# Performance work log

Hardware: AMD Instinct MI355X
Metric: run time of the kernel (lower is better)

## Reference

```python
import jax, jax.numpy as jnp
import numpy as np
import math
from jax import lax


def _pos_enc(C, T, V, dtype):
    # spatial positional encoding: position = joint index j for every (t, j)
    pos = jnp.tile(jnp.arange(V, dtype=dtype), T)[:, None]            # (T*V, 1)
    div = jnp.exp(jnp.arange(0, C, 2, dtype=dtype) * (-(math.log(10000.0) / C)))
    ang = pos * div                                                   # (T*V, C//2)
    pe = jnp.stack([jnp.sin(ang), jnp.cos(ang)], axis=-1).reshape(T * V, C)
    return pe.reshape(T, V, C).transpose(2, 0, 1)[None]               # (1, C, T, V)


def _sparsemax(z, axis):
    z = jnp.moveaxis(z, axis, -1)
    K = z.shape[-1]
    zs = jnp.flip(jnp.sort(z, axis=-1), axis=-1)                      # descending
    cs = jnp.cumsum(zs, axis=-1)
    k = jnp.arange(1, K + 1, dtype=z.dtype)
    support = (1.0 + k * zs) > cs
    ks = jnp.sum(support, axis=-1, keepdims=True)                     # support size (int)
    tau = (jnp.take_along_axis(cs, ks - 1, axis=-1) - 1.0) / ks.astype(z.dtype)
    out = jnp.maximum(z - tau, 0.0)
    return jnp.moveaxis(out, -1, axis)


def _conv2d(x, w, b, pad_h=0, stride_h=1):
    out = lax.conv_general_dilated(x, w, (stride_h, 1), ((pad_h, pad_h), (0, 0)),
                                   dimension_numbers=('NCHW', 'OIHW', 'NCHW'))
    return out + b.reshape(1, -1, 1, 1)


def _bn(x, g, be, m, v, eps=1e-5):
    inv = g / jnp.sqrt(v + eps)
    return x * inv.reshape(1, -1, 1, 1) + (be - m * inv).reshape(1, -1, 1, 1)


def reference(x, theta, atts, alphas, v_w, v_b, out_w, out_b, out_g, out_be, out_m, out_v,
              ff_w, ff_b, ff_g, ff_be, ff_m, ff_v):
    N, C, T, V = x.shape
    S = theta.shape[1]

    # positional encoding + kernel attention
    y = x + _pos_enc(C, T, V, x.dtype)
    yf = y.transpose(0, 3, 1, 2).reshape(N, V, C * T)                 # (N, V, C*T)
    sq = jnp.sum(yf * yf, axis=-1)
    d2 = sq[:, :, None] + sq[:, None, :] - 2.0 * jnp.einsum('nvd,nud->nvu', yf, yf)
    d2 = jnp.maximum(d2, 0.0)                                         # cdist^2
    dism = d2 / float((C * T) ** 2)                                   # (d / (C*T))^2
    dism = dism / jnp.max(dism)
    kernel_atten = jnp.exp(-jnp.exp(theta) * dism[:, None])           # (N, S, V, V)
    kernel_atten = _sparsemax(kernel_atten, axis=-2)                  # sparsity_alpha == 2
    attention = atts + kernel_atten * alphas                          # is_regularization=True; dropout in eval

    # value mapping (1x1 conv) + subset aggregation
    vx = jnp.einsum('oc,nctv->notv', v_w.reshape(v_w.shape[0], v_w.shape[1]), x) + v_b.reshape(1, -1, 1, 1)
    y = jnp.einsum('nctu,nsuv->nsctv', vx, attention).reshape(N, S * C, T, V)

    # out_nets: temporal conv (k,1) + BN
    pad = (out_w.shape[2] - 1) // 2
    y = _bn(_conv2d(y, out_w, out_b, pad_h=pad), out_g, out_be, out_m, out_v)
    y = jax.nn.leaky_relu(x + y, negative_slope=0.1)                  # downs1 = identity

    # ff_nets: 1x1 conv + BN
    y2 = _bn(_conv2d(y, ff_w, ff_b), ff_g, ff_be, ff_m, ff_v)
    return jax.nn.leaky_relu(x + y2, negative_slope=0.1)              # downs2 = identity


def setup_inputs() -> dict:
    key = jax.random.key(0)
    ks = jax.random.split(key, 8)
    N, C, T, V, S, K = 64, 128, 128, 25, 3, 7
    Cout = 128
    inp = {}
    inp['x'] = jax.random.normal(ks[0], (N, C, T, V), dtype=jnp.float32)
    inp['theta'] = jax.random.normal(ks[1], (1, S, 1, 1), dtype=jnp.float32) * 0.1
    inp['atts'] = jax.random.normal(ks[2], (1, S, V, V), dtype=jnp.float32) * 0.1
    inp['alphas'] = jnp.ones((1, S, 1, 1), dtype=jnp.float32)
    inp['v_w'] = jax.random.normal(ks[3], (C, C, 1, 1), dtype=jnp.float32) * (1.0 / math.sqrt(C))
    inp['v_b'] = jax.random.normal(ks[4], (C,), dtype=jnp.float32) * 0.01
    inp['out_w'] = jax.random.normal(ks[5], (Cout, S * C, K, 1), dtype=jnp.float32) * (1.0 / math.sqrt(S * C * K))
    inp['out_b'] = jax.random.normal(ks[6], (Cout,), dtype=jnp.float32) * 0.01
    inp['out_g'] = jnp.ones((Cout,), dtype=jnp.float32)
    inp['out_be'] = jnp.zeros((Cout,), dtype=jnp.float32)
    inp['out_m'] = jnp.zeros((Cout,), dtype=jnp.float32)
    inp['out_v'] = jnp.ones((Cout,), dtype=jnp.float32)
    inp['ff_w'] = jax.random.normal(ks[7], (Cout, Cout, 1, 1), dtype=jnp.float32) * (1.0 / math.sqrt(Cout))
    inp['ff_b'] = jnp.zeros((Cout,), dtype=jnp.float32)
    inp['ff_g'] = jnp.ones((Cout,), dtype=jnp.float32)
    inp['ff_be'] = jnp.zeros((Cout,), dtype=jnp.float32)
    inp['ff_m'] = jnp.zeros((Cout,), dtype=jnp.float32)
    inp['ff_v'] = jnp.ones((Cout,), dtype=jnp.float32)
    return inp
```

## Files before the change

### kernel.cpp

```cpp
#include <hip/hip_runtime.h>
#include <hip/hip_bf16.h>
#include <math.h>

typedef __attribute__((ext_vector_type(8))) short s16x8;
typedef __attribute__((ext_vector_type(4))) float f32x4;

static __device__ __forceinline__ float bf2f(unsigned short u){
    unsigned int x = ((unsigned int)u) << 16; float f; __builtin_memcpy(&f,&x,4); return f;
}
static __device__ __forceinline__ unsigned short f2bf(float f){
    unsigned int x; __builtin_memcpy(&x,&f,4);
    unsigned int r = (x + 0x7FFFu + ((x>>16)&1u)) >> 16; return (unsigned short)r;
}

static __device__ __forceinline__ void stage16(const void* g, void* l){
    __builtin_amdgcn_global_load_lds((const __attribute__((address_space(1))) unsigned int*)g,
                                     (__attribute__((address_space(3))) unsigned int*)l, 16, 0, 0);
}


__global__ __launch_bounds__(256) void setup_kernel(const float* __restrict__ x,
                            const float* __restrict__ out_w, const float* __restrict__ ff_w,
                            const float* __restrict__ v_w,  const float* __restrict__ v_b,
                            const float* __restrict__ out_b, const float* __restrict__ out_g,
                            const float* __restrict__ out_be, const float* __restrict__ out_m,
                            const float* __restrict__ out_v,
                            const float* __restrict__ ff_b, const float* __restrict__ ff_g,
                            const float* __restrict__ ff_be, const float* __restrict__ ff_m,
                            const float* __restrict__ ff_v,
                            float* __restrict__ consts, unsigned short* __restrict__ ffA,
                            unsigned short* __restrict__ ypad, float* __restrict__ wbpart,
                            float* __restrict__ pebg, float* __restrict__ TPgb,
                            unsigned short* __restrict__ Wr,
                            unsigned short* __restrict__ xbt, unsigned short* __restrict__ xbu,
                            float* __restrict__ G, float* __restrict__ SX)
{
    __shared__ float tile[64][65];
    const int bid = blockIdx.x;
    const int tid = threadIdx.x;

    if (bid < 6400){
        int jb = bid % 50; int cb = (bid/50) & 1; int n = bid/100;
        int lane = tid & 63, wv = tid >> 6;
        size_t xbase = (size_t)n*409600;
        int jn = jb*64 + lane;
        int tt = jn/25, uu = jn - tt*25;
        size_t xbu_lb = (size_t)n*524288 + (size_t)tt*4096 + uu;
        #pragma unroll
        for (int r=wv; r<64; r+=4){
            float v = x[xbase + (size_t)(cb*64+r)*3200 + jb*64 + lane];
            tile[r][lane] = v;
            xbu[xbu_lb + (size_t)(cb*64+r)*32] = f2bf(v);
        }
        __syncthreads();
        #pragma unroll
        for (int j=wv; j<64; j+=4)
            xbt[xbase + (size_t)(jb*64+j)*128 + cb*64 + lane] = f2bf(tile[lane][j]);
        return;
    }

    if (bid < 7296){
        float* owl = &tile[0][0];
        int wb = bid - 6400;
        int o = wb/7, k = wb%7;
        for (int i=tid; i<384; i+=256) owl[i] = out_w[(size_t)(o*384 + i)*7 + k];
        __syncthreads();
        for (int sci=tid; sci<384; sci+=256){
            int s = sci >> 7, ci = sci & 127;
            const float* ow = owl + s*128;
            float acc = 0.f;
            #pragma unroll 8
            for (int c=0; c<128; ++c) acc += ow[c] * v_w[c*128 + ci];
            int kb = (sci>>5)*7 + k, jj = sci & 31;
            Wr[(size_t)o*2688 + kb*32 + jj] = f2bf(acc);
        }
        return;
    }

    const int stride = 2048*256;
    int i0 = (bid-7296)*256 + tid;
    const float KLN = 9.210340371976184f/128.f;
    for (int i=i0; i<40000;  i+=stride) G[i]  = 0.f;
    for (int i=i0; i<204800; i+=stride) SX[i] = 0.f;
    for (int i=i0; i<16384; i+=stride) ffA[i] = f2bf(ff_w[i]);
    for (int i=i0; i<128; i+=stride){
        float inv  = out_g[i]/sqrtf(out_v[i]+1e-5f);
        consts[i]       = inv;
        consts[128+i]   = out_b[i]*inv + out_be[i] - out_m[i]*inv;
        float invf = ff_g[i]/sqrtf(ff_v[i]+1e-5f);
        consts[256+i]   = invf;
        consts[384+i]   = ff_b[i]*invf + ff_be[i] - ff_m[i]*invf;
    }
    for (int i=i0; i<3200; i+=stride){
        int v = i >> 7, c = i & 127;
        float freq = expf(-(float)(c & ~1) * KLN);
        float ang = (float)v * freq;
        pebg[i] = (c & 1) ? cosf(ang) : sinf(ang);
    }
    for (int i=i0; i<625; i+=stride){
        int u = i/25, v = i%25;
        float acc = 0.f;
        for (int c=0; c<128; ++c){
            float freq = expf(-(float)(c & ~1) * KLN);
            float pu = (c & 1) ? cosf((float)u*freq) : sinf((float)u*freq);
            float pv = (c & 1) ? cosf((float)v*freq) : sinf((float)v*freq);
            acc += pu*pv;
        }
        TPgb[i] = 128.f*acc;
    }
    for (int i=i0; i<2688; i+=stride){
        int o = i/21, rem = i%21, s = rem/7, tc = rem%7;
        int kmin = (tc<3) ? (3-tc) : 0;
        int kmax = (tc>3) ? (10-tc) : 7;
        float acc = 0.f;
        for (int c=0; c<128; ++c){
            const float* wp = out_w + (size_t)(o*384 + s*128 + c)*7;
            float vb = v_b[c];
            for (int k=kmin; k<kmax; ++k) acc += wp[k]*vb;
        }
        wbpart[i] = acc;
    }
    for (int i=i0; i<3686400; i+=stride){
        int n2 = i/57600, r2 = i%57600;
        int pp = r2/384, sc = r2%384;
        int ppos = (pp < 75) ? pp : (3200 + pp);
        ypad[(size_t)(n2*3350 + ppos)*384 + sc] = 0;
    }
}

__global__ __launch_bounds__(256) void gram_part(const unsigned short* __restrict__ xbt,
                                                 float* __restrict__ G, float* __restrict__ SX){
    __shared__ float glx[4][32][32];
    int bid = blockIdx.x; int n = bid >> 3; int chunk = bid & 7;
    int tid = threadIdx.x;
    const unsigned short* xb = xbt + (size_t)n*409600;

    int c = tid & 127, th = tid >> 7;
    float a[25];
    #pragma unroll
    for (int u=0; u<25; ++u) a[u] = 0.f;
    for (int tt=0; tt<8; ++tt){
        int t = chunk*16 + th*8 + tt;
        const unsigned short* row = xb + (size_t)t*3200 + c;
        #pragma unroll
        for (int u=0; u<25; ++u) a[u] += bf2f(row[u*128]);
    }
    float* tmp = &glx[0][0][0];
    if (th){
        #pragma unroll
        for (int u=0; u<25; ++u) tmp[u*128+c] = a[u];
    }
    __syncthreads();
    if (!th){
        #pragma unroll
        for (int u=0; u<25; ++u) atomicAdd(&SX[n*3200 + u*128 + c], a[u] + tmp[u*128+c]);
    }
    __syncthreads();

    int lane = tid & 63, w = tid >> 6;
    int lr = lane & 15, lg = lane >> 4;
    f32x4 acc[2][2];
    #pragma unroll
    for (int i2=0;i2<2;i2++)
        #pragma unroll
        for (int j2=0;j2<2;j2++) acc[i2][j2] = (f32x4){0.f,0.f,0.f,0.f};
    for (int tt=0; tt<4; ++tt){
        int t = chunk*16 + w*4 + tt;
        const unsigned short* tb = xb + (size_t)t*3200;
        #pragma unroll
        for (int kc=0; kc<4; ++kc){
            s16x8 f0 = *(const s16x8*)(tb + (size_t)(lr)*128    + kc*32 + lg*8);
            s16x8 f1 = *(const s16x8*)(tb + (size_t)(16+lr)*128 + kc*32 + lg*8);
            acc[0][0] = __builtin_amdgcn_mfma_f32_16x16x32_bf16(f0, f0, acc[0][0], 0,0,0);
            acc[0][1] = __builtin_amdgcn_mfma_f32_16x16x32_bf16(f0, f1, acc[0][1], 0,0,0);
            acc[1][0] = __builtin_amdgcn_mfma_f32_16x16x32_bf16(f1, f0, acc[1][0], 0,0,0);
            acc[1][1] = __builtin_amdgcn_mfma_f32_16x16x32_bf16(f1, f1, acc[1][1], 0,0,0);
        }
    }
    #pragma unroll
    for (int mh=0; mh<2; ++mh)
        #pragma unroll
        for (int nh=0; nh<2; ++nh)
            #pragma unroll
            for (int r=0; r<4; ++r)
                glx[w][mh*16 + lg*4 + r][nh*16 + lr] = acc[mh][nh][r];
    __syncthreads();
    for (int idx=tid; idx<625; idx+=256){
        int u = idx/25, v = idx%25;
        atomicAdd(&G[n*625 + idx], glx[0][u][v] + glx[1][u][v] + glx[2][u][v] + glx[3][u][v]);
    }
}

__global__ __launch_bounds__(256) void gram_fin(const float* __restrict__ SX,
                                                const float* __restrict__ pebg,
                                                const float* __restrict__ TPgb,
                                                float* __restrict__ G,
                                                float* __restrict__ nmax){
    __shared__ float sxl[25][129];
    __shared__ float pebl[25][129];
    __shared__ float gf[625];
    __shared__ float red[256];
    int n = blockIdx.x, tid = threadIdx.x;
    for (int i=tid; i<3200; i+=256){
        sxl[i>>7][i&127]  = SX[n*3200 + i];
        pebl[i>>7][i&127] = pebg[i];
    }
    __syncthreads();
    for (int idx=tid; idx<625; idx+=256){
        int u = idx/25, v = idx%25;
        float cr = TPgb[idx];
        #pragma unroll 4
        for (int cc=0; cc<128; ++cc)
            cr += sxl[u][cc]*pebl[v][cc] + sxl[v][cc]*pebl[u][cc];
        float val = G[n*625 + idx] + cr;
        G[n*625 + idx] = val;
        gf[idx] = val;
    }
    __syncthreads();
    float mx = 0.f;
    for (int idx=tid; idx<625; idx+=256){
        int u = idx/25, v = idx%25;
        float d2 = fmaxf(gf[u*26] + gf[v*26] - 2.f*gf[u*25+v], 0.f);
        mx = fmaxf(mx, d2);
    }
    red[tid] = mx; __syncthreads();
    for (int s2=128; s2>0; s2>>=1){ if (tid < s2) red[tid] = fmaxf(red[tid], red[tid+s2]); __syncthreads(); }
    if (tid == 0) nmax[n] = red[0];
}

__global__ __launch_bounds__(128) void attn_kernel(const float* __restrict__ G, const float* __restrict__ nmax,
                                                   const float* __restrict__ theta,
                                                   const float* __restrict__ atts, const float* __restrict__ alphas,
                                                   unsigned short* __restrict__ att_pad, float* __restrict__ asum){
    __shared__ float gl[625];
    __shared__ float red[64];
    int n = blockIdx.x, tid = threadIdx.x;
    if (tid < 64) red[tid] = nmax[tid];
    for (int i=tid; i<625; i+=128) gl[i] = G[n*625 + i];
    __syncthreads();
    if (tid == 0){
        float m = red[0];
        for (int i=1; i<64; ++i) m = fmaxf(m, red[i]);
        red[0] = m;
    }
    __syncthreads();
    float inv = 1.f/red[0];
    for (int i=tid; i<160; i+=128) att_pad[n*2560 + 2400 + i] = 0;
    if (tid < 75){
        int s = tid/25, vc = tid%25;
        float et = expf(theta[s]);
        float al = alphas[s];
        float gvv = gl[vc*26];
        float z[25];
        #pragma unroll
        for (int u2=0; u2<25; ++u2){
            float d2v = fmaxf(gl[u2*26] + gvv - 2.f*gl[u2*25+vc], 0.f);
            z[u2] = expf(-et*d2v*inv);
        }
        float zm = z[0];
        #pragma unroll
        for (int u2=1; u2<25; ++u2) zm = fmaxf(zm, z[u2]);
        float lo = zm - 1.f, hi = zm;
        for (int it=0; it<30; ++it){
            float mid = 0.5f*(lo+hi);
            float f = 0.f;
            #pragma unroll
            for (int u2=0; u2<25; ++u2) f += fmaxf(z[u2]-mid, 0.f);
            if (f >= 1.f) lo = mid; else hi = mid;
        }
        float ssum = 0.f; int kcnt = 0;
        #pragma unroll
        for (int u2=0; u2<25; ++u2){ if (z[u2] > lo){ ssum += z[u2]; kcnt++; } }
        float tau = (ssum - 1.f)/(float)kcnt;
        float as_ = 0.f;
        unsigned short* apr = att_pad + n*2560 + (s*25+vc)*32;
        #pragma unroll
        for (int u2=0; u2<25; ++u2){
            float av = atts[s*625 + u2*25 + vc] + fmaxf(z[u2]-tau, 0.f)*al;
            apr[u2] = f2bf(av);
            as_ += av;
        }
        #pragma unroll
        for (int u2=25; u2<32; ++u2) apr[u2] = 0;
        asum[n*75 + s*25 + vc] = as_;
    }
}

__global__ __launch_bounds__(256,2) void agg_mfma(const unsigned short* __restrict__ att_pad,
                                                  const unsigned short* __restrict__ xbu,
                                                  unsigned short* __restrict__ ypad){
    int bid = blockIdx.x; int n = bid >> 4; int tb = bid & 15;
    int tid = threadIdx.x; int lane = tid & 63; int w = tid >> 6;
    int lr = lane & 15, lg = lane >> 4;
    const unsigned short* ap = att_pad + n*2560;
    s16x8 a[5];
    #pragma unroll
    for (int mf=0; mf<5; ++mf) a[mf] = *(const s16x8*)&ap[(mf*16+lr)*32 + lg*8];
    int rowoff[5][4];
    #pragma unroll
    for (int mf=0; mf<5; ++mf)
        #pragma unroll
        for (int r=0; r<4; ++r){
            int m = mf*16 + lg*4 + r;
            int s = m/25, v = m - s*25;
            rowoff[mf][r] = (m < 75) ? (v*384 + s*128 + lr) : -1;
        }
    #pragma unroll
    for (int ti=0; ti<2; ++ti){
        int t = tb*8 + w*2 + ti;
        const unsigned short* bp = xbu + (size_t)n*524288 + (size_t)t*4096;
        size_t obase = ((size_t)(n*3350 + 75 + t*25))*384;
        #pragma unroll
        for (int h=0; h<2; ++h){
            s16x8 b[4];
            #pragma unroll
            for (int q=0; q<4; ++q){
                b[q] = *(const s16x8*)&bp[(h*64 + q*16 + lr)*32 + lg*8];
                if (lg == 3){
                    s16x8 t2 = b[q];
                    b[q] = (s16x8){t2[0],0,0,0,0,0,0,0};
                }
            }
            f32x4 acc[5][4];
            #pragma unroll
            for (int mf=0; mf<5; ++mf)
                #pragma unroll
                for (int q=0; q<4; ++q)
                    acc[mf][q] = (f32x4){0.f,0.f,0.f,0.f};
            #pragma unroll
            for (int mf=0; mf<5; ++mf)
                #pragma unroll
                for (int q=0; q<4; ++q)
                    acc[mf][q] = __builtin_amdgcn_mfma_f32_16x16x32_bf16(a[mf], b[q], acc[mf][q], 0, 0, 0);
            #pragma unroll
            for (int mf=0; mf<5; ++mf)
                #pragma unroll
                for (int q=0; q<4; ++q)
                    #pragma unroll
                    for (int r=0; r<4; ++r)
                        if (rowoff[mf][r] >= 0)
                            ypad[obase + rowoff[mf][r] + h*64 + q*16] = f2bf(acc[mf][q][r]);
        }
    }
}

__global__ __launch_bounds__(256,3) void gemm_fused(const unsigned short* __restrict__ Amat,
                                                    const unsigned short* __restrict__ Bsrc,
                                                    const float* __restrict__ xin,
                                                    const float* __restrict__ consts,
                                                    const unsigned short* __restrict__ ffA,
                                                    const float* __restrict__ wbpart,
                                                    const float* __restrict__ asum,
                                                    float* __restrict__ outf)
{
    constexpr int NKB = 42;
    __shared__ unsigned short smem[17560];

    const int tid = threadIdx.x;
    const int bid = blockIdx.x;
    const int n   = bid/25;
    const int jn0 = (bid%25)*128;

    const int lane = tid & 63, wv = tid >> 6;
    const int wm = wv >> 1, wn = wv & 1;
    const int lr = lane & 15, lg = lane >> 4;

    unsigned short* sA = smem;
    unsigned short* sB = smem + 8192;

    auto stage = [&](int kb){
        #pragma unroll
        for (int p=0; p<4; ++p){
            int e = p*256 + tid;
            int r = e >> 3, cch = e & 7;
            int cc8 = cch ^ (r & 7);
            stage16(Amat + (size_t)r*2688 + kb*64 + cc8*8, sA + e*8);
        }
        int k32a = 2*kb, k32b = 2*kb + 1;
        int k0 = k32a % 7, s0 = (k32a/7)*32;
        int k1 = k32b % 7, s1 = (k32b/7)*32;
        const unsigned short* b0 = Bsrc + ((size_t)(n*3350 + jn0 + 25*k0))*384 + s0;
        const unsigned short* b1 = Bsrc + ((size_t)(n*3350 + jn0 + 25*k1))*384 + s1;
        #pragma unroll
        for (int p=0; p<4; ++p){
            int e = p*256 + tid;
            int r = e >> 3, cch = e & 7;
            int cc8 = cch ^ (r & 7);
            const unsigned short* src = ((cc8 >> 2) ? b1 : b0) + (size_t)r*384 + (cc8&3)*8;
            stage16(src, sB + e*8);
        }
    };

    f32x4 acc[4][4];
    #pragma unroll
    for (int a2=0;a2<4;a2++)
        #pragma unroll
        for (int b2=0;b2<4;b2++) acc[a2][b2] = (f32x4){0.f,0.f,0.f,0.f};

    for (int kb=0; kb<NKB; ++kb){
        stage(kb);
        __syncthreads();
        s16x8 a[4][2], b[4][2];
        #pragma unroll
        for (int mf=0; mf<4; ++mf)
            #pragma unroll
            for (int kf=0; kf<2; ++kf)
                a[mf][kf] = *(const s16x8*)&sA[(wm*64+mf*16+lr)*64 + (((kf*4+lg) ^ (lr&7))<<3)];
        #pragma unroll
        for (int nf=0; nf<4; ++nf)
            #pragma unroll
            for (int kf=0; kf<2; ++kf)
                b[nf][kf] = *(const s16x8*)&sB[(wn*64+nf*16+lr)*64 + (((kf*4+lg) ^ (lr&7))<<3)];
        __builtin_amdgcn_s_setprio(1);
        #pragma unroll
        for (int kf=0; kf<2; ++kf)
            #pragma unroll
            for (int mf=0; mf<4; ++mf)
                #pragma unroll
                for (int nf=0; nf<4; ++nf)
                    acc[mf][nf] = __builtin_amdgcn_mfma_f32_16x16x32_bf16(a[mf][kf], b[nf][kf], acc[mf][nf], 0, 0, 0);
        __builtin_amdgcn_s_setprio(0);
        __syncthreads();
    }

    float* asl = (float*)(smem + 17408);
    for (int i=tid; i<75; i+=256) asl[i] = asum[n*75 + i];
    __syncthreads();

    #pragma unroll
    for (int nf=0; nf<4; ++nf){
        int cj = wn*64 + nf*16 + lr;
        int j  = jn0 + cj;
        int t  = j/25, v = j - t*25;
        int tc = (t<3) ? t : ((t>124) ? (t-121) : 3);
        float a0 = asl[v], a1 = asl[25+v], a2 = asl[50+v];
        #pragma unroll
        for (int mf=0; mf<4; ++mf)
            #pragma unroll
            for (int r=0; r<4; ++r){
                int m = wm*64 + mf*16 + lg*4 + r;
                float b2v = wbpart[m*21+tc]*a0 + wbpart[m*21+7+tc]*a1 + wbpart[m*21+14+tc]*a2;
                float val = acc[mf][nf][r]*consts[m] + consts[128+m] + b2v
                          + xin[(size_t)n*409600 + (size_t)m*3200 + j];
                val = (val >= 0.f) ? val : 0.1f*val;
                smem[cj*136 + m] = f2bf(val);
            }
    }
    __syncthreads();

    f32x4 acc2[4][4];
    #pragma unroll
    for (int a2=0;a2<4;a2++)
        #pragma unroll
        for (int b2=0;b2<4;b2++) acc2[a2][b2] = (f32x4){0.f,0.f,0.f,0.f};
    #pragma unroll
    for (int kb2=0; kb2<4; ++kb2){
        s16x8 a2[4], b2[4];
        #pragma unroll
        for (int mf=0; mf<4; ++mf)
            a2[mf] = *(const s16x8*)&ffA[(size_t)(wm*64+mf*16+lr)*128 + kb2*32 + lg*8];
        #pragma unroll
        for (int nf=0; nf<4; ++nf)
            b2[nf] = *(const s16x8*)&smem[(wn*64+nf*16+lr)*136 + kb2*32 + lg*8];
        #pragma unroll
        for (int mf=0; mf<4; ++mf)
            #pragma unroll
            for (int nf=0; nf<4; ++nf)
                acc2[mf][nf] = __builtin_amdgcn_mfma_f32_16x16x32_bf16(a2[mf], b2[nf], acc2[mf][nf], 0, 0, 0);
    }

    #pragma unroll
    for (int mf=0; mf<4; ++mf)
        #pragma unroll
        for (int r=0; r<4; ++r){
            int co = wm*64 + mf*16 + lg*4 + r;
            float sc2 = consts[256+co], bi2 = consts[384+co];
            #pragma unroll
            for (int nf=0; nf<4; ++nf){
                int cj = wn*64 + nf*16 + lr;
                size_t idx = (size_t)n*409600 + (size_t)co*3200 + jn0 + cj;
                float val = acc2[mf][nf][r]*sc2 + bi2 + xin[idx];
                val = (val >= 0.f) ? val : 0.1f*val;
                outf[idx] = val;
            }
        }
}

extern "C" void kernel_launch(void* const* d_in, const int* in_sizes, int n_in,
                              void* d_out, int out_size, void* d_ws, size_t ws_size,
                              hipStream_t stream) {
    const float* x      = (const float*)d_in[0];
    const float* theta  = (const float*)d_in[1];
    const float* atts   = (const float*)d_in[2];
    const float* alphas = (const float*)d_in[3];
    const float* v_w    = (const float*)d_in[4];
    const float* v_b    = (const float*)d_in[5];
    const float* out_w  = (const float*)d_in[6];
    const float* out_b  = (const float*)d_in[7];
    const float* out_g  = (const float*)d_in[8];
    const float* out_be = (const float*)d_in[9];
    const float* out_m  = (const float*)d_in[10];
    const float* out_v  = (const float*)d_in[11];
    const float* ff_w   = (const float*)d_in[12];
    const float* ff_b   = (const float*)d_in[13];
    const float* ff_g   = (const float*)d_in[14];
    const float* ff_be  = (const float*)d_in[15];
    const float* ff_m   = (const float*)d_in[16];
    const float* ff_v   = (const float*)d_in[17];
    float* out = (float*)d_out;

    char* w = (char*)d_ws;
    size_t off = 0;
    auto alloc = [&](size_t b){ size_t r = off; off += (b + 1023) & ~(size_t)1023; return r; };
    float*          G      = (float*)         (w + alloc(160000));
    float*          SX     = (float*)         (w + alloc(819200));
    float*          nmaxb  = (float*)         (w + alloc(256));
    float*          asumb  = (float*)         (w + alloc(19200));
    float*          consts = (float*)         (w + alloc(2048));
    float*          wbpart = (float*)         (w + alloc(10752));
    float*          pebg   = (float*)         (w + alloc(12800));
    float*          TPgb   = (float*)         (w + alloc(2500));
    unsigned short* att_pad= (unsigned short*)(w + alloc(327680));
    unsigned short* Wr     = (unsigned short*)(w + alloc(688128));
    unsigned short* ffA    = (unsigned short*)(w + alloc(32768));
    unsigned short* xbt    = (unsigned short*)(w + alloc(52428800 + 16384));
    unsigned short* xbu    = (unsigned short*)(w + alloc(67108864));
    unsigned short* ypad   = (unsigned short*)(w + alloc(164659200));

    setup_kernel<<<9344,256,0,stream>>>(x, out_w, ff_w, v_w, v_b, out_b, out_g, out_be, out_m, out_v,
                                        ff_b, ff_g, ff_be, ff_m, ff_v,
                                        consts, ffA, ypad, wbpart, pebg, TPgb, Wr, xbt, xbu, G, SX);
    gram_part<<<512,256,0,stream>>>(xbt, G, SX);
    gram_fin<<<64,256,0,stream>>>(SX, pebg, TPgb, G, nmaxb);
    attn_kernel<<<64,128,0,stream>>>(G, nmaxb, theta, atts, alphas, att_pad, asumb);
    agg_mfma<<<1024,256,0,stream>>>(att_pad, xbu, ypad);
    gemm_fused<<<1600,256,0,stream>>>(Wr, ypad, x, consts, ffA, wbpart, asumb, out);
}
```

Before: 492.7 us.

## Load MFMA operands directly from global memory instead of staging through LDS

The GEMM main loop stops staging A and B tiles into shared memory with global_load_lds and barriers. Each lane now loads its MFMA fragments straight from global memory into registers, and the loop is unrolled by two. This removes LDS traffic and the two __syncthreads per k-step. In exchange, operands that the four waves used to share through LDS are now fetched from global memory redundantly, which relies on L1/L2 hits, and the loads are less coalesced (16-byte chunks spread across strided rows).

New measurement: 833.0 us. +69.1%, slower.

```diff
diff --git a/kernel.cpp b/kernel.cpp
--- a/kernel.cpp
+++ b/kernel.cpp
@@ -365,31 +365,15 @@
     const int wm = wv >> 1, wn = wv & 1;
     const int lr = lane & 15, lg = lane >> 4;
 
-    unsigned short* sA = smem;
-    unsigned short* sB = smem + 8192;
-
-    auto stage = [&](int kb){
-        #pragma unroll
-        for (int p=0; p<4; ++p){
-            int e = p*256 + tid;
-            int r = e >> 3, cch = e & 7;
-            int cc8 = cch ^ (r & 7);
-            stage16(Amat + (size_t)r*2688 + kb*64 + cc8*8, sA + e*8);
-        }
-        int k32a = 2*kb, k32b = 2*kb + 1;
-        int k0 = k32a % 7, s0 = (k32a/7)*32;
-        int k1 = k32b % 7, s1 = (k32b/7)*32;
-        const unsigned short* b0 = Bsrc + ((size_t)(n*3350 + jn0 + 25*k0))*384 + s0;
-        const unsigned short* b1 = Bsrc + ((size_t)(n*3350 + jn0 + 25*k1))*384 + s1;
-        #pragma unroll
-        for (int p=0; p<4; ++p){
-            int e = p*256 + tid;
-            int r = e >> 3, cch = e & 7;
-            int cc8 = cch ^ (r & 7);
-            const unsigned short* src = ((cc8 >> 2) ? b1 : b0) + (size_t)r*384 + (cc8&3)*8;
-            stage16(src, sB + e*8);
-        }
-    };
+    const unsigned short* aptr0 = Amat + (size_t)(wm*64 + 0*16 + lr)*2688 + lg*8;
+    const unsigned short* aptr1 = Amat + (size_t)(wm*64 + 1*16 + lr)*2688 + lg*8;
+    const unsigned short* aptr2 = Amat + (size_t)(wm*64 + 2*16 + lr)*2688 + lg*8;
+    const unsigned short* aptr3 = Amat + (size_t)(wm*64 + 3*16 + lr)*2688 + lg*8;
+    const size_t brow0 = (size_t)(wn*64 + 0*16 + lr)*384 + lg*8;
+    const size_t brow1 = (size_t)(wn*64 + 1*16 + lr)*384 + lg*8;
+    const size_t brow2 = (size_t)(wn*64 + 2*16 + lr)*384 + lg*8;
+    const size_t brow3 = (size_t)(wn*64 + 3*16 + lr)*384 + lg*8;
+    const unsigned short* Bbase = Bsrc + (size_t)(n*3350 + jn0)*384;
 
     f32x4 acc[4][4];
     #pragma unroll
@@ -397,20 +381,23 @@
         #pragma unroll
         for (int b2=0;b2<4;b2++) acc[a2][b2] = (f32x4){0.f,0.f,0.f,0.f};
 
+    #pragma unroll 2
     for (int kb=0; kb<NKB; ++kb){
-        stage(kb);
-        __syncthreads();
         s16x8 a[4][2], b[4][2];
         #pragma unroll
-        for (int mf=0; mf<4; ++mf)
-            #pragma unroll
-            for (int kf=0; kf<2; ++kf)
-                a[mf][kf] = *(const s16x8*)&sA[(wm*64+mf*16+lr)*64 + (((kf*4+lg) ^ (lr&7))<<3)];
-        #pragma unroll
-        for (int nf=0; nf<4; ++nf)
-            #pragma unroll
-            for (int kf=0; kf<2; ++kf)
-                b[nf][kf] = *(const s16x8*)&sB[(wn*64+nf*16+lr)*64 + (((kf*4+lg) ^ (lr&7))<<3)];
+        for (int kf=0; kf<2; ++kf){
+            int k32 = 2*kb + kf;
+            int k = k32 % 7, scb = (k32/7)*32;
+            const unsigned short* bp = Bbase + (size_t)(25*k)*384 + scb;
+            a[0][kf] = *(const s16x8*)(aptr0 + k32*32);
+            a[1][kf] = *(const s16x8*)(aptr1 + k32*32);
+            a[2][kf] = *(const s16x8*)(aptr2 + k32*32);
+            a[3][kf] = *(const s16x8*)(aptr3 + k32*32);
+            b[0][kf] = *(const s16x8*)(bp + brow0);
+            b[1][kf] = *(const s16x8*)(bp + brow1);
+            b[2][kf] = *(const s16x8*)(bp + brow2);
+            b[3][kf] = *(const s16x8*)(bp + brow3);
+        }
         __builtin_amdgcn_s_setprio(1);
         #pragma unroll
         for (int kf=0; kf<2; ++kf)
@@ -420,7 +407,6 @@
                 for (int nf=0; nf<4; ++nf)
                     acc[mf][nf] = __builtin_amdgcn_mfma_f32_16x16x32_bf16(a[mf][kf], b[nf][kf], acc[mf][nf], 0, 0, 0);
         __builtin_amdgcn_s_setprio(0);
-        __syncthreads();
     }
 
     float* asl = (float*)(smem + 17408);
```
